# Kernel optimization log

Measured on AMD Instinct MI355X. Metric: run time of the kernel, lower is better.

## Reference

```python
import jax, jax.numpy as jnp
import numpy as np
from functools import partial

B = 524288
DIM = 2
COND = 64
HID = 64
STEPS = 10


def setup_inputs() -> dict:
    key = jax.random.key(0)
    ks = jax.random.split(key, 8)
    in_dim = DIM + COND + 1  # z, context, t feature
    return {
        "x": jax.random.normal(ks[0], (B, DIM), jnp.float32),
        "context": jax.random.normal(ks[1], (B, COND), jnp.float32),
        # fresh Hutchinson noise per RK4 substep: (steps-1) intervals x 4 stages
        "eps": jax.random.normal(ks[2], (STEPS - 1, 4, B, DIM), jnp.float32),
        "W1": jax.random.normal(ks[3], (in_dim, HID), jnp.float32) * 0.1,
        "b1": jnp.zeros((HID,), jnp.float32),
        "W2": jax.random.normal(ks[4], (HID, HID), jnp.float32) * 0.1,
        "b2": jnp.zeros((HID,), jnp.float32),
        "W3": jax.random.normal(ks[5], (HID, DIM), jnp.float32) * 0.1,
        "b3": jnp.zeros((DIM,), jnp.float32),
        "steps": STEPS,
    }


def _mlp(h, W1, b1, W2, b2, W3, b3):
    h = jnp.tanh(h @ W1 + b1)
    h = jnp.tanh(h @ W2 + b2)
    return h @ W3 + b3


def reference(x, context, eps, W1, b1, W2, b2, W3, b3, steps):
    params = (W1, b1, W2, b2, W3, b3)
    dtype = x.dtype

    def f_net(z, t):
        tfeat = jnp.full((z.shape[0], 1), 1.0, dtype) * t  # [B,1]
        return _mlp(jnp.concatenate([z, context, tfeat], axis=1), *params)

    def func(t, z, eps_k):
        # f and Hutchinson divergence estimate eps^T (df/dz) eps via one vjp
        f, vjp_fn = jax.vjp(lambda zz: f_net(zz, t), z)
        (g,) = vjp_fn(eps_k)  # eps^T J, shape [B, DIM]
        div = jnp.sum(g * eps_k, axis=1, keepdims=True)  # [B,1]
        return f, -div

    tspan = jnp.linspace(1.0, 0.0, steps, dtype=dtype)  # t0=1.0 -> t1=0.0
    z0 = x
    lp0 = jnp.zeros((x.shape[0], 1), dtype)

    def step(carry, xs):
        z, lp = carry
        ti, tf, e4 = xs  # e4: [4, B, DIM]
        h = tf - ti
        k1z, k1l = func(ti, z, e4[0])
        k2z, k2l = func(ti + 0.5 * h, z + 0.5 * h * k1z, e4[1])
        k3z, k3l = func(ti + 0.5 * h, z + 0.5 * h * k2z, e4[2])
        k4z, k4l = func(tf, z + h * k3z, e4[3])
        zn = z + h / 6.0 * (k1z + 2.0 * k2z + 2.0 * k3z + k4z)
        lpn = lp + h / 6.0 * (k1l + 2.0 * k2l + 2.0 * k3l + k4l)
        return (zn, lpn), None

    (z1, lp1), _ = jax.lax.scan(step, (z0, lp0), (tspan[:-1], tspan[1:], eps))
    return z1, lp1
```

## Files before the change

kernel.cpp:

```cpp
#include <hip/hip_runtime.h>
#include <cstddef>

typedef __attribute__((__ext_vector_type__(8))) short bf16x8;
typedef __attribute__((__ext_vector_type__(4))) float f32x4;

#define MFMA16(a, b, c) __builtin_amdgcn_mfma_f32_16x16x32_bf16((a), (b), (c), 0, 0, 0)

__device__ __forceinline__ unsigned short bf16_rne(float f) {
    unsigned int u = __float_as_uint(f);
    u += 0x7fffu + ((u >> 16) & 1u);
    return (unsigned short)(u >> 16);
}
__device__ __forceinline__ float bf16_to_f32(unsigned short h) {
    return __uint_as_float(((unsigned int)h) << 16);
}
__device__ __forceinline__ float tanh_fast(float x) {
    float e = __expf(2.f * x);
    return __builtin_fmaf(-2.f, __builtin_amdgcn_rcpf(e + 1.f), 1.f);
}
__device__ __forceinline__ unsigned int pk_bf16(float lo, float hi) {
    unsigned int r;
    asm("v_cvt_pk_bf16_f32 %0, %1, %2" : "=v"(r) : "v"(lo), "v"(hi));
    return r;
}

__global__ __launch_bounds__(256, 3)
void cnf_mfma_kernel(const float* __restrict__ x,
                     const float* __restrict__ ctx,
                     const float* __restrict__ eps,
                     const float* __restrict__ W1,
                     const float* __restrict__ b1,
                     const float* __restrict__ W2,
                     const float* __restrict__ b2,
                     const float* __restrict__ W3,
                     const float* __restrict__ b3,
                     float* __restrict__ out,
                     int nb)
{
    __shared__ __align__(16) unsigned short sW2f[4096];
    __shared__ __align__(16) unsigned short lds[4 * 32 * 72];

    const int tid  = threadIdx.x;
    const int lane = tid & 63;
    const int wv   = tid >> 6;
    const int l15  = lane & 15;
    const int quad = lane >> 4;
    unsigned short* tbH = &lds[wv * 32 * 72];
    unsigned short* tbT = tbH + 16 * 72;

    for (int idx = tid; idx < 4096; idx += 256) {
        int i = idx >> 6, c = idx & 63;
        int kp = (i & 15) * 4 + (i >> 4);
        sW2f[(((kp >> 5) * 4 + (c >> 4)) * 64 + ((kp >> 3) & 3) * 16 + (c & 15)) * 8 + (kp & 7)] =
            bf16_rne(W2[idx]);
    }
    __syncthreads();

    const int sBase = (blockIdx.x * 4 + wv) * 16;
    if (sBase >= nb) return;

    float w1z0[4], w1z1[4], w1tt[4], b2c[4], w30c[4], w31c[4];
    #pragma unroll
    for (int t = 0; t < 4; ++t) {
        int col = t * 16 + l15;
        w1z0[t] = W1[col];
        w1z1[t] = W1[64 + col];
        w1tt[t] = W1[66 * 64 + col];
        b2c[t]  = b2[col];
        w30c[t] = W3[2 * col];
        w31c[t] = W3[2 * col + 1];
    }
    const float b30 = b3[0], b31 = b3[1];

    f32x4 c1[4];
    {
        bf16x8 ah[2], al[2];
        #pragma unroll
        for (int ks = 0; ks < 2; ++ks) {
            bf16x8 h_, l_;
            #pragma unroll
            for (int j = 0; j < 8; ++j) {
                float v = ctx[(size_t)(sBase + l15) * 64 + ks * 32 + quad * 8 + j];
                unsigned short hh = bf16_rne(v);
                h_[j] = (short)hh;
                l_[j] = (short)bf16_rne(v - bf16_to_f32(hh));
            }
            ah[ks] = h_; al[ks] = l_;
        }
        #pragma unroll
        for (int t = 0; t < 4; ++t) {
            f32x4 acc;
            float b1c = b1[t * 16 + l15];
            acc[0] = b1c; acc[1] = b1c; acc[2] = b1c; acc[3] = b1c;
            #pragma unroll
            for (int ks = 0; ks < 2; ++ks) {
                bf16x8 bh, bl;
                #pragma unroll
                for (int j = 0; j < 8; ++j) {
                    float v = W1[(size_t)(2 + ks * 32 + quad * 8 + j) * 64 + t * 16 + l15];
                    unsigned short hh = bf16_rne(v);
                    bh[j] = (short)hh;
                    bl[j] = (short)bf16_rne(v - bf16_to_f32(hh));
                }
                acc = MFMA16(ah[ks], bh, acc);
                acc = MFMA16(al[ks], bh, acc);
                acc = MFMA16(ah[ks], bl, acc);
            }
            c1[t] = acc;
        }
    }

    float z0[4], z1[4], lp[4];
    #pragma unroll
    for (int r = 0; r < 4; ++r) {
        z0[r] = x[(size_t)(sBase + quad * 4 + r) * 2];
        z1[r] = x[(size_t)(sBase + quad * 4 + r) * 2 + 1];
        lp[r] = 0.f;
    }

    const float hstep = -1.f / 9.f;

    float e0c[4], e1c[4], e0n[4], e1n[4];
    {
        const float* p = eps + (size_t)(sBase + quad * 4) * 2;
        #pragma unroll
        for (int r = 0; r < 4; ++r) { e0c[r] = p[2 * r]; e1c[r] = p[2 * r + 1]; }
    }

    #pragma unroll 1
    for (int k = 0; k < 9; ++k) {
        float ti = 1.f + (float)k * hstep;
        float ze0[4], ze1[4], zs0[4], zs1[4], lsum[4];
        #pragma unroll
        for (int r = 0; r < 4; ++r) {
            ze0[r] = z0[r]; ze1[r] = z1[r];
            zs0[r] = 0.f; zs1[r] = 0.f; lsum[r] = 0.f;
        }

        #pragma unroll 1
        for (int st = 0; st < 4; ++st) {
            int zo = 0;
            __asm__ volatile("" : "+v"(zo));
            const unsigned short* pf = sW2f + zo;

            float coef = (st == 0) ? 0.f : ((st == 3) ? 1.f : 0.5f);
            float tcur = ti + coef * hstep;
            int stg = k * 4 + st;
            if (stg < 35) {
                const float* p = eps + ((size_t)(stg + 1) * (size_t)nb + sBase + quad * 4) * 2;
                #pragma unroll
                for (int r = 0; r < 4; ++r) { e0n[r] = p[2 * r]; e1n[r] = p[2 * r + 1]; }
            }

            __asm__ volatile("s_waitcnt lgkmcnt(0)" ::: "memory");

            #pragma unroll
            for (int r = 0; r < 4; ++r) {
                float hf[4], tf[4];
                #pragma unroll
                for (int t = 0; t < 4; ++t) {
                    float pre = c1[t][r];
                    pre = __builtin_fmaf(ze0[r], w1z0[t], pre);
                    pre = __builtin_fmaf(ze1[r], w1z1[t], pre);
                    pre = __builtin_fmaf(tcur,  w1tt[t], pre);
                    float h = tanh_fast(pre);
                    hf[t] = h;
                    float ew = __builtin_fmaf(e1c[r], w1z1[t], e0c[r] * w1z0[t]);
                    tf[t] = ew * __builtin_fmaf(-h, h, 1.f);
                }
                uint2 hw, tw;
                hw.x = pk_bf16(hf[0], hf[1]); hw.y = pk_bf16(hf[2], hf[3]);
                tw.x = pk_bf16(tf[0], tf[1]); tw.y = pk_bf16(tf[2], tf[3]);
                *(uint2*)&tbH[(quad * 4 + r) * 72 + l15 * 4] = hw;
                *(uint2*)&tbT[(quad * 4 + r) * 72 + l15 * 4] = tw;
            }
            __asm__ volatile("s_waitcnt lgkmcnt(0)" ::: "memory");
            bf16x8 a1k0 = *(const bf16x8*)&tbH[l15 * 72 + quad * 8];
            bf16x8 a1k1 = *(const bf16x8*)&tbH[l15 * 72 + 32 + quad * 8];
            bf16x8 atk0 = *(const bf16x8*)&tbT[l15 * 72 + quad * 8];
            bf16x8 atk1 = *(const bf16x8*)&tbT[l15 * 72 + 32 + quad * 8];

            float f0p[4] = {0.f, 0.f, 0.f, 0.f};
            float f1p[4] = {0.f, 0.f, 0.f, 0.f};
            float dvp[4] = {0.f, 0.f, 0.f, 0.f};
            #pragma unroll
            for (int t = 0; t < 4; ++t) {
                bf16x8 bk0 = *(const bf16x8*)&pf[(t * 64 + lane) * 8];
                bf16x8 bk1 = *(const bf16x8*)&pf[((4 + t) * 64 + lane) * 8];
                f32x4 af; af[0] = b2c[t]; af[1] = b2c[t]; af[2] = b2c[t]; af[3] = b2c[t];
                af = MFMA16(a1k0, bk0, af);
                af = MFMA16(a1k1, bk1, af);
                f32x4 at_; at_[0] = 0.f; at_[1] = 0.f; at_[2] = 0.f; at_[3] = 0.f;
                at_ = MFMA16(atk0, bk0, at_);
                at_ = MFMA16(atk1, bk1, at_);
                #pragma unroll
                for (int r = 0; r < 4; ++r) {
                    float h2 = tanh_fast(af[r]);
                    f0p[r] = __builtin_fmaf(h2, w30c[t], f0p[r]);
                    f1p[r] = __builtin_fmaf(h2, w31c[t], f1p[r]);
                    float td2 = __builtin_fmaf(-h2, h2, 1.f);
                    float t2v = at_[r] * td2;
                    float ew3 = __builtin_fmaf(e1c[r], w31c[t], e0c[r] * w30c[t]);
                    dvp[r] = __builtin_fmaf(t2v, ew3, dvp[r]);
                }
            }

            #pragma unroll
            for (int m = 1; m < 16; m <<= 1) {
                #pragma unroll
                for (int r = 0; r < 4; ++r) {
                    f0p[r] += __shfl_xor(f0p[r], m, 16);
                    f1p[r] += __shfl_xor(f1p[r], m, 16);
                    dvp[r] += __shfl_xor(dvp[r], m, 16);
                }
            }

            float wgt = (st == 1 || st == 2) ? 2.f : 1.f;
            #pragma unroll
            for (int r = 0; r < 4; ++r) {
                float f0 = f0p[r] + b30;
                float f1 = f1p[r] + b31;
                zs0[r]  = __builtin_fmaf(wgt, f0, zs0[r]);
                zs1[r]  = __builtin_fmaf(wgt, f1, zs1[r]);
                lsum[r] = __builtin_fmaf(wgt, -dvp[r], lsum[r]);
                if (st < 3) {
                    float cn = (st == 2) ? 1.f : 0.5f;
                    ze0[r] = __builtin_fmaf(cn * hstep, f0, z0[r]);
                    ze1[r] = __builtin_fmaf(cn * hstep, f1, z1[r]);
                }
                e0c[r] = e0n[r]; e1c[r] = e1n[r];
            }
        }

        const float h6 = hstep * (1.f / 6.f);
        #pragma unroll
        for (int r = 0; r < 4; ++r) {
            z0[r] = __builtin_fmaf(h6, zs0[r], z0[r]);
            z1[r] = __builtin_fmaf(h6, zs1[r], z1[r]);
            lp[r] = __builtin_fmaf(h6, lsum[r], lp[r]);
        }
    }

    if (l15 == 0) {
        #pragma unroll
        for (int r = 0; r < 4; ++r) {
            int s = sBase + quad * 4 + r;
            out[2 * s]     = z0[r];
            out[2 * s + 1] = z1[r];
            out[2 * nb + s] = lp[r];
        }
    }
}

extern "C" void kernel_launch(void* const* d_in, const int* in_sizes, int n_in,
                              void* d_out, int out_size, void* d_ws, size_t ws_size,
                              hipStream_t stream) {
    const float* x   = (const float*)d_in[0];
    const float* ctx = (const float*)d_in[1];
    const float* eps = (const float*)d_in[2];
    const float* W1  = (const float*)d_in[3];
    const float* b1  = (const float*)d_in[4];
    const float* W2  = (const float*)d_in[5];
    const float* b2  = (const float*)d_in[6];
    const float* W3  = (const float*)d_in[7];
    const float* b3  = (const float*)d_in[8];
    float* out = (float*)d_out;

    int nb = in_sizes[0] / 2;
    int grid = (nb + 63) / 64;
    hipLaunchKernelGGL(cnf_mfma_kernel, dim3(grid), dim3(256), 0, stream,
                       x, ctx, eps, W1, b1, W2, b2, W3, b3, out, nb);
}
```

Before: 1.585 ms.

## Pack elementwise math into float2 FMAs, use DPP reductions, defer divergence reduction

Rewrites the per-row elementwise work (layer-1 preactivation, tanh, tangent, layer-3 accumulation, RK4 updates) with two-wide packed fp32 FMAs, and uses raw v_exp_f32 with a folded 2*log2e constant. Replaces the shuffle-based 16-lane reductions with DPP adds. The divergence is kept as per-lane partials (split by eps component) that are accumulated across all steps and reduced only once at the end, which relies on linearity. Eps loads become float4 vector loads with a pointer increment. The aim is fewer VALU instructions and cross-lane operations in the inner loop, at the cost of more registers.

Result: faster. 1.444 ms (-8.9%).

```diff
diff --git a/kernel.cpp b/kernel.cpp
--- a/kernel.cpp
+++ b/kernel.cpp
@@ -3,6 +3,7 @@
 
 typedef __attribute__((__ext_vector_type__(8))) short bf16x8;
 typedef __attribute__((__ext_vector_type__(4))) float f32x4;
+typedef __attribute__((__ext_vector_type__(2))) float f32x2;
 
 #define MFMA16(a, b, c) __builtin_amdgcn_mfma_f32_16x16x32_bf16((a), (b), (c), 0, 0, 0)
 
@@ -14,15 +15,44 @@
 __device__ __forceinline__ float bf16_to_f32(unsigned short h) {
     return __uint_as_float(((unsigned int)h) << 16);
 }
-__device__ __forceinline__ float tanh_fast(float x) {
-    float e = __expf(2.f * x);
-    return __builtin_fmaf(-2.f, __builtin_amdgcn_rcpf(e + 1.f), 1.f);
-}
 __device__ __forceinline__ unsigned int pk_bf16(float lo, float hi) {
     unsigned int r;
     asm("v_cvt_pk_bf16_f32 %0, %1, %2" : "=v"(r) : "v"(lo), "v"(hi));
     return r;
 }
+__device__ __forceinline__ float exp2_raw(float x) {
+    float r;
+    asm("v_exp_f32 %0, %1" : "=v"(r) : "v"(x));
+    return r;
+}
+__device__ __forceinline__ f32x2 pk_fma(f32x2 a, f32x2 b, f32x2 c) {
+    return __builtin_elementwise_fma(a, b, c);
+}
+__device__ __forceinline__ f32x2 tanh_pair(f32x2 x) {
+    const f32x2 k2l2e = {2.88539008177793f, 2.88539008177793f};
+    f32x2 t = x * k2l2e;
+    f32x2 e;
+    e.x = exp2_raw(t.x);
+    e.y = exp2_raw(t.y);
+    f32x2 ep1 = e + (f32x2){1.f, 1.f};
+    f32x2 r;
+    r.x = __builtin_amdgcn_rcpf(ep1.x);
+    r.y = __builtin_amdgcn_rcpf(ep1.y);
+    return pk_fma((f32x2){-2.f, -2.f}, r, (f32x2){1.f, 1.f});
+}
+template <int CTRL>
+__device__ __forceinline__ float dpp_add(float v) {
+    int t = __builtin_amdgcn_update_dpp(0, __float_as_int(v), CTRL, 0xF, 0xF, false);
+    return v + __int_as_float(t);
+}
+__device__ __forceinline__ float allred16(float v) {
+    v = dpp_add<0xB1>(v);
+    v = dpp_add<0x4E>(v);
+    v = dpp_add<0x124>(v);
+    v = dpp_add<0x128>(v);
+    return v;
+}
+__device__ __forceinline__ float vc(f32x2 v, int c) { return c ? v.y : v.x; }
 
 __global__ __launch_bounds__(256, 3)
 void cnf_mfma_kernel(const float* __restrict__ x,
@@ -59,20 +89,23 @@
     const int sBase = (blockIdx.x * 4 + wv) * 16;
     if (sBase >= nb) return;
 
-    float w1z0[4], w1z1[4], w1tt[4], b2c[4], w30c[4], w31c[4];
+    f32x2 w1z0d[4], w1z1d[4], w1ttd[4], w30d[4], w31d[4];
+    float b2c[4];
     #pragma unroll
     for (int t = 0; t < 4; ++t) {
         int col = t * 16 + l15;
-        w1z0[t] = W1[col];
-        w1z1[t] = W1[64 + col];
-        w1tt[t] = W1[66 * 64 + col];
-        b2c[t]  = b2[col];
-        w30c[t] = W3[2 * col];
-        w31c[t] = W3[2 * col + 1];
+        float a0 = W1[col], a1 = W1[64 + col], a2 = W1[66 * 64 + col];
+        float a3 = W3[2 * col], a4 = W3[2 * col + 1];
+        w1z0d[t] = (f32x2){a0, a0};
+        w1z1d[t] = (f32x2){a1, a1};
+        w1ttd[t] = (f32x2){a2, a2};
+        w30d[t]  = (f32x2){a3, a3};
+        w31d[t]  = (f32x2){a4, a4};
+        b2c[t]   = b2[col];
     }
     const float b30 = b3[0], b31 = b3[1];
 
-    f32x4 c1[4];
+    f32x2 c1h[4][2];
     {
         bf16x8 ah[2], al[2];
         #pragma unroll
@@ -106,35 +139,41 @@
                 acc = MFMA16(al[ks], bh, acc);
                 acc = MFMA16(ah[ks], bl, acc);
             }
-            c1[t] = acc;
-        }
-    }
-
-    float z0[4], z1[4], lp[4];
+            c1h[t][0] = (f32x2){acc[0], acc[1]};
+            c1h[t][1] = (f32x2){acc[2], acc[3]};
+        }
+    }
+
+    f32x2 z0p[2], z1p[2], lsump[2];
     #pragma unroll
-    for (int r = 0; r < 4; ++r) {
-        z0[r] = x[(size_t)(sBase + quad * 4 + r) * 2];
-        z1[r] = x[(size_t)(sBase + quad * 4 + r) * 2 + 1];
-        lp[r] = 0.f;
+    for (int rp = 0; rp < 2; ++rp) {
+        const float* px = x + (size_t)(sBase + quad * 4 + rp * 2) * 2;
+        z0p[rp] = (f32x2){px[0], px[2]};
+        z1p[rp] = (f32x2){px[1], px[3]};
+        lsump[rp] = (f32x2){0.f, 0.f};
     }
 
     const float hstep = -1.f / 9.f;
 
-    float e0c[4], e1c[4], e0n[4], e1n[4];
+    f32x2 e0p[2], e1p[2], e0np[2] = {{0.f,0.f},{0.f,0.f}}, e1np[2] = {{0.f,0.f},{0.f,0.f}};
     {
         const float* p = eps + (size_t)(sBase + quad * 4) * 2;
-        #pragma unroll
-        for (int r = 0; r < 4; ++r) { e0c[r] = p[2 * r]; e1c[r] = p[2 * r + 1]; }
-    }
+        float4 q0 = *(const float4*)(p);
+        float4 q1 = *(const float4*)(p + 4);
+        e0p[0] = (f32x2){q0.x, q0.z}; e1p[0] = (f32x2){q0.y, q0.w};
+        e0p[1] = (f32x2){q1.x, q1.z}; e1p[1] = (f32x2){q1.y, q1.w};
+    }
+    const float* ep = eps + ((size_t)nb + sBase + quad * 4) * 2;
+    const size_t estride = (size_t)nb * 2;
 
     #pragma unroll 1
     for (int k = 0; k < 9; ++k) {
         float ti = 1.f + (float)k * hstep;
-        float ze0[4], ze1[4], zs0[4], zs1[4], lsum[4];
-        #pragma unroll
-        for (int r = 0; r < 4; ++r) {
-            ze0[r] = z0[r]; ze1[r] = z1[r];
-            zs0[r] = 0.f; zs1[r] = 0.f; lsum[r] = 0.f;
+        f32x2 ze0p[2], ze1p[2], zs0p[2], zs1p[2];
+        #pragma unroll
+        for (int rp = 0; rp < 2; ++rp) {
+            ze0p[rp] = z0p[rp]; ze1p[rp] = z1p[rp];
+            zs0p[rp] = (f32x2){0.f, 0.f}; zs1p[rp] = (f32x2){0.f, 0.f};
         }
 
         #pragma unroll 1
@@ -145,34 +184,43 @@
 
             float coef = (st == 0) ? 0.f : ((st == 3) ? 1.f : 0.5f);
             float tcur = ti + coef * hstep;
+            f32x2 tcur2 = (f32x2){tcur, tcur};
             int stg = k * 4 + st;
             if (stg < 35) {
-                const float* p = eps + ((size_t)(stg + 1) * (size_t)nb + sBase + quad * 4) * 2;
-                #pragma unroll
-                for (int r = 0; r < 4; ++r) { e0n[r] = p[2 * r]; e1n[r] = p[2 * r + 1]; }
-            }
+                float4 q0 = *(const float4*)(ep);
+                float4 q1 = *(const float4*)(ep + 4);
+                e0np[0] = (f32x2){q0.x, q0.z}; e1np[0] = (f32x2){q0.y, q0.w};
+                e0np[1] = (f32x2){q1.x, q1.z}; e1np[1] = (f32x2){q1.y, q1.w};
+            }
+            ep += estride;
 
             __asm__ volatile("s_waitcnt lgkmcnt(0)" ::: "memory");
 
             #pragma unroll
-            for (int r = 0; r < 4; ++r) {
-                float hf[4], tf[4];
+            for (int rp = 0; rp < 2; ++rp) {
+                f32x2 hv[4], tv[4];
                 #pragma unroll
                 for (int t = 0; t < 4; ++t) {
-                    float pre = c1[t][r];
-                    pre = __builtin_fmaf(ze0[r], w1z0[t], pre);
-                    pre = __builtin_fmaf(ze1[r], w1z1[t], pre);
-                    pre = __builtin_fmaf(tcur,  w1tt[t], pre);
-                    float h = tanh_fast(pre);
-                    hf[t] = h;
-                    float ew = __builtin_fmaf(e1c[r], w1z1[t], e0c[r] * w1z0[t]);
-                    tf[t] = ew * __builtin_fmaf(-h, h, 1.f);
-                }
-                uint2 hw, tw;
-                hw.x = pk_bf16(hf[0], hf[1]); hw.y = pk_bf16(hf[2], hf[3]);
-                tw.x = pk_bf16(tf[0], tf[1]); tw.y = pk_bf16(tf[2], tf[3]);
-                *(uint2*)&tbH[(quad * 4 + r) * 72 + l15 * 4] = hw;
-                *(uint2*)&tbT[(quad * 4 + r) * 72 + l15 * 4] = tw;
+                    f32x2 pre = c1h[t][rp];
+                    pre = pk_fma(ze0p[rp], w1z0d[t], pre);
+                    pre = pk_fma(ze1p[rp], w1z1d[t], pre);
+                    pre = pk_fma(tcur2, w1ttd[t], pre);
+                    f32x2 h = tanh_pair(pre);
+                    hv[t] = h;
+                    f32x2 ew = pk_fma(e1p[rp], w1z1d[t], e0p[rp] * w1z0d[t]);
+                    tv[t] = ew * pk_fma(-h, h, (f32x2){1.f, 1.f});
+                }
+                #pragma unroll
+                for (int c = 0; c < 2; ++c) {
+                    int row = quad * 4 + rp * 2 + c;
+                    uint2 hw, tw;
+                    hw.x = pk_bf16(vc(hv[0], c), vc(hv[1], c));
+                    hw.y = pk_bf16(vc(hv[2], c), vc(hv[3], c));
+                    tw.x = pk_bf16(vc(tv[0], c), vc(tv[1], c));
+                    tw.y = pk_bf16(vc(tv[2], c), vc(tv[3], c));
+                    *(uint2*)&tbH[row * 72 + l15 * 4] = hw;
+                    *(uint2*)&tbT[row * 72 + l15 * 4] = tw;
+                }
             }
             __asm__ volatile("s_waitcnt lgkmcnt(0)" ::: "memory");
             bf16x8 a1k0 = *(const bf16x8*)&tbH[l15 * 72 + quad * 8];
@@ -180,9 +228,8 @@
             bf16x8 atk0 = *(const bf16x8*)&tbT[l15 * 72 + quad * 8];
             bf16x8 atk1 = *(const bf16x8*)&tbT[l15 * 72 + 32 + quad * 8];
 
-            float f0p[4] = {0.f, 0.f, 0.f, 0.f};
-            float f1p[4] = {0.f, 0.f, 0.f, 0.f};
-            float dvp[4] = {0.f, 0.f, 0.f, 0.f};
+            f32x2 f0pp[2] = {{0.f,0.f},{0.f,0.f}}, f1pp[2] = {{0.f,0.f},{0.f,0.f}};
+            f32x2 dv0pp[2] = {{0.f,0.f},{0.f,0.f}}, dv1pp[2] = {{0.f,0.f},{0.f,0.f}};
             #pragma unroll
             for (int t = 0; t < 4; ++t) {
                 bf16x8 bk0 = *(const bf16x8*)&pf[(t * 64 + lane) * 8];
@@ -194,60 +241,73 @@
                 at_ = MFMA16(atk0, bk0, at_);
                 at_ = MFMA16(atk1, bk1, at_);
                 #pragma unroll
-                for (int r = 0; r < 4; ++r) {
-                    float h2 = tanh_fast(af[r]);
-                    f0p[r] = __builtin_fmaf(h2, w30c[t], f0p[r]);
-                    f1p[r] = __builtin_fmaf(h2, w31c[t], f1p[r]);
-                    float td2 = __builtin_fmaf(-h2, h2, 1.f);
-                    float t2v = at_[r] * td2;
-                    float ew3 = __builtin_fmaf(e1c[r], w31c[t], e0c[r] * w30c[t]);
-                    dvp[r] = __builtin_fmaf(t2v, ew3, dvp[r]);
-                }
-            }
-
-            #pragma unroll
-            for (int m = 1; m < 16; m <<= 1) {
-                #pragma unroll
-                for (int r = 0; r < 4; ++r) {
-                    f0p[r] += __shfl_xor(f0p[r], m, 16);
-                    f1p[r] += __shfl_xor(f1p[r], m, 16);
-                    dvp[r] += __shfl_xor(dvp[r], m, 16);
-                }
+                for (int rp = 0; rp < 2; ++rp) {
+                    f32x2 afp = rp ? (f32x2){af[2], af[3]} : (f32x2){af[0], af[1]};
+                    f32x2 atp = rp ? (f32x2){at_[2], at_[3]} : (f32x2){at_[0], at_[1]};
+                    f32x2 h2 = tanh_pair(afp);
+                    f0pp[rp] = pk_fma(h2, w30d[t], f0pp[rp]);
+                    f1pp[rp] = pk_fma(h2, w31d[t], f1pp[rp]);
+                    f32x2 t2v = atp * pk_fma(-h2, h2, (f32x2){1.f, 1.f});
+                    dv0pp[rp] = pk_fma(t2v, w30d[t], dv0pp[rp]);
+                    dv1pp[rp] = pk_fma(t2v, w31d[t], dv1pp[rp]);
+                }
+            }
+
+            #pragma unroll
+            for (int rp = 0; rp < 2; ++rp) {
+                f0pp[rp].x = allred16(f0pp[rp].x);
+                f0pp[rp].y = allred16(f0pp[rp].y);
+                f1pp[rp].x = allred16(f1pp[rp].x);
+                f1pp[rp].y = allred16(f1pp[rp].y);
             }
 
             float wgt = (st == 1 || st == 2) ? 2.f : 1.f;
-            #pragma unroll
-            for (int r = 0; r < 4; ++r) {
-                float f0 = f0p[r] + b30;
-                float f1 = f1p[r] + b31;
-                zs0[r]  = __builtin_fmaf(wgt, f0, zs0[r]);
-                zs1[r]  = __builtin_fmaf(wgt, f1, zs1[r]);
-                lsum[r] = __builtin_fmaf(wgt, -dvp[r], lsum[r]);
+            f32x2 wgt2 = (f32x2){wgt, wgt};
+            f32x2 wgtn2 = (f32x2){-wgt, -wgt};
+            float cn = (st == 2) ? 1.f : 0.5f;
+            f32x2 ch2 = (f32x2){cn * hstep, cn * hstep};
+            #pragma unroll
+            for (int rp = 0; rp < 2; ++rp) {
+                f32x2 f0 = f0pp[rp] + (f32x2){b30, b30};
+                f32x2 f1 = f1pp[rp] + (f32x2){b31, b31};
+                zs0p[rp] = pk_fma(wgt2, f0, zs0p[rp]);
+                zs1p[rp] = pk_fma(wgt2, f1, zs1p[rp]);
+                f32x2 nd = pk_fma(dv1pp[rp], e1p[rp], dv0pp[rp] * e0p[rp]);
+                lsump[rp] = pk_fma(nd, wgtn2, lsump[rp]);
                 if (st < 3) {
-                    float cn = (st == 2) ? 1.f : 0.5f;
-                    ze0[r] = __builtin_fmaf(cn * hstep, f0, z0[r]);
-                    ze1[r] = __builtin_fmaf(cn * hstep, f1, z1[r]);
-                }
-                e0c[r] = e0n[r]; e1c[r] = e1n[r];
+                    ze0p[rp] = pk_fma(ch2, f0, z0p[rp]);
+                    ze1p[rp] = pk_fma(ch2, f1, z1p[rp]);
+                }
+                e0p[rp] = e0np[rp]; e1p[rp] = e1np[rp];
             }
         }
 
         const float h6 = hstep * (1.f / 6.f);
-        #pragma unroll
-        for (int r = 0; r < 4; ++r) {
-            z0[r] = __builtin_fmaf(h6, zs0[r], z0[r]);
-            z1[r] = __builtin_fmaf(h6, zs1[r], z1[r]);
-            lp[r] = __builtin_fmaf(h6, lsum[r], lp[r]);
-        }
-    }
+        f32x2 h62 = (f32x2){h6, h6};
+        #pragma unroll
+        for (int rp = 0; rp < 2; ++rp) {
+            z0p[rp] = pk_fma(h62, zs0p[rp], z0p[rp]);
+            z1p[rp] = pk_fma(h62, zs1p[rp], z1p[rp]);
+        }
+    }
+
+    const float h6f = hstep * (1.f / 6.f);
+    float lpv[4];
+    lpv[0] = h6f * allred16(lsump[0].x);
+    lpv[1] = h6f * allred16(lsump[0].y);
+    lpv[2] = h6f * allred16(lsump[1].x);
+    lpv[3] = h6f * allred16(lsump[1].y);
 
     if (l15 == 0) {
         #pragma unroll
-        for (int r = 0; r < 4; ++r) {
-            int s = sBase + quad * 4 + r;
-            out[2 * s]     = z0[r];
-            out[2 * s + 1] = z1[r];
-            out[2 * nb + s] = lp[r];
+        for (int rp = 0; rp < 2; ++rp) {
+            int s = sBase + quad * 4 + rp * 2;
+            out[2 * s]       = z0p[rp].x;
+            out[2 * s + 1]   = z1p[rp].x;
+            out[2 * s + 2]   = z0p[rp].y;
+            out[2 * s + 3]   = z1p[rp].y;
+            out[2 * nb + s]     = lpv[rp * 2];
+            out[2 * nb + s + 1] = lpv[rp * 2 + 1];
         }
     }
 }
```
